# Kernel optimization log

Hardware: AMD Instinct MI355X
Metric: run time of the kernel (lower is better)

## Reference

```python
import jax, jax.numpy as jnp
import numpy as np

D_MODEL = 2048
H = 16
D_K = D_MODEL // H


def setup_inputs() -> dict:
    key = jax.random.key(0)
    ks = jax.random.split(key, 9)
    b, n, d = 2, 2048, D_MODEL
    s = 1.0 / np.sqrt(d)
    return {
        "x": jax.random.normal(ks[0], (b, n, d), jnp.float32),
        "Wq": jax.random.normal(ks[1], (d, d), jnp.float32) * s,
        "bq": jax.random.normal(ks[2], (d,), jnp.float32) * 0.01,
        "Wk": jax.random.normal(ks[3], (d, d), jnp.float32) * s,
        "bk": jax.random.normal(ks[4], (d,), jnp.float32) * 0.01,
        "Wv": jax.random.normal(ks[5], (d, d), jnp.float32) * s,
        "bv": jax.random.normal(ks[6], (d,), jnp.float32) * 0.01,
        "Wo": jax.random.normal(ks[7], (d, d), jnp.float32) * s,
        "bo": jax.random.normal(ks[8], (d,), jnp.float32) * 0.01,
    }


def reference(x, Wq, bq, Wk, bk, Wv, bv, Wo, bo):
    b, n, d = x.shape
    h, dk = H, D_K

    def split_heads(t):
        return t.reshape(b, n, h, dk).transpose(0, 2, 1, 3)  # (b,h,n,dk)

    q = split_heads(x @ Wq + bq)
    k = split_heads(x @ Wk + bk)
    v = split_heads(x @ Wv + bv)

    scores = jnp.einsum("bhqd,bhkd->bhqk", q, k) / jnp.sqrt(jnp.float32(dk))
    causal = jnp.tril(jnp.ones((n, n), dtype=bool))  # (n,n)
    scores = jnp.where(causal[None, None], scores, -jnp.inf)
    attn = jax.nn.softmax(scores, axis=-1)  # dropout = identity (eval)

    out = jnp.einsum("bhqk,bhkd->bhqd", attn, v)
    out = out.transpose(0, 2, 1, 3).reshape(b, n, d)
    return out @ Wo + bo
```

## Files before the change

kernel.cpp:

```cpp
#include <hip/hip_runtime.h>

typedef unsigned short u16;
typedef unsigned int u32;
typedef __attribute__((ext_vector_type(8))) short short8;
typedef __attribute__((ext_vector_type(4))) float f32x4;
typedef __attribute__((ext_vector_type(16))) float f32x16;
typedef __attribute__((ext_vector_type(4))) u16 u16x4;
typedef __attribute__((ext_vector_type(4))) u32 u32x4;

#define QK_SCALE 0.12751736915185197f

__device__ __forceinline__ u16 f2bf(float f) {
  u32 u = __builtin_bit_cast(u32, f);
  u = u + 0x7FFFu + ((u >> 16) & 1u);
  return (u16)(u >> 16);
}

__device__ __forceinline__ void async_copy16(const void* g, void* l) {
  __builtin_amdgcn_global_load_lds(
      (const __attribute__((address_space(1))) u32*)g,
      (__attribute__((address_space(3))) u32*)l, 16, 0, 0);
}

#define VMCNT(n) asm volatile("s_waitcnt vmcnt(" #n ")" ::: "memory")

__global__ __launch_bounds__(256) void cast_x_kernel(const float* __restrict__ x,
                                                     u16* __restrict__ xb, int n) {
  int i = (blockIdx.x * 256 + threadIdx.x) * 8;
  if (i >= n) return;
  float4 a = *(const float4*)(x + i);
  float4 b = *(const float4*)(x + i + 4);
  short8 o;
  o[0] = (short)f2bf(a.x); o[1] = (short)f2bf(a.y);
  o[2] = (short)f2bf(a.z); o[3] = (short)f2bf(a.w);
  o[4] = (short)f2bf(b.x); o[5] = (short)f2bf(b.y);
  o[6] = (short)f2bf(b.z); o[7] = (short)f2bf(b.w);
  *(short8*)(xb + i) = o;
}

__global__ __launch_bounds__(256) void transW_kernel(
    const float* __restrict__ W0, const float* __restrict__ W1,
    const float* __restrict__ W2, const float* __restrict__ W3,
    u16* __restrict__ O0, u16* __restrict__ O1, u16* __restrict__ O2, u16* __restrict__ O3) {
  const float* Ws[4] = {W0, W1, W2, W3};
  u16* Os[4] = {O0, O1, O2, O3};
  const float* W = Ws[blockIdx.z];
  u16* O = Os[blockIdx.z];

  __shared__ float T[64][65];
  int t = threadIdx.x;
  int k0 = blockIdx.y * 64, n0 = blockIdx.x * 64;
  int r = t >> 4, c = (t & 15) * 4;
#pragma unroll
  for (int i = 0; i < 4; ++i) {
    float4 v = *(const float4*)&W[(size_t)(k0 + r + i * 16) * 2048 + n0 + c];
    T[r + i * 16][c + 0] = v.x; T[r + i * 16][c + 1] = v.y;
    T[r + i * 16][c + 2] = v.z; T[r + i * 16][c + 3] = v.w;
  }
  __syncthreads();
#pragma unroll
  for (int i = 0; i < 4; ++i) {
    int nn = r + i * 16;
    u16x4 o;
    o[0] = f2bf(T[c + 0][nn]); o[1] = f2bf(T[c + 1][nn]);
    o[2] = f2bf(T[c + 2][nn]); o[3] = f2bf(T[c + 3][nn]);
    *(u16x4*)&O[(size_t)(n0 + nn) * 2048 + k0 + c] = o;
  }
}

__global__ __launch_bounds__(512, 2) void gemm192_kernel(
    const u16* __restrict__ A, const u16* __restrict__ W,
    const float* __restrict__ b0, const float* __restrict__ b1, const float* __restrict__ b2,
    u16* __restrict__ oq, u16* __restrict__ ok, u16* __restrict__ ovt) {
  __shared__ __align__(16) u16 SM[57344];

  int t = threadIdx.x;
  int lane = t & 63, w = t >> 6;
  int wm = w >> 2, wn = w & 3;
  int g = lane >> 4, lr = lane & 15;
  int m0 = blockIdx.y * 256, n0 = blockIdx.x * 192;

  const u16* AsrcB = A + (size_t)(m0 + (t >> 3)) * 2048 + ((t & 7) ^ ((t >> 3) & 7)) * 8;
  const u16* BsrcB = W + (size_t)(n0 + (t >> 3)) * 2048 + ((t & 7) ^ ((t >> 3) & 7)) * 8;
  int t8 = t * 8;

  int ko0 = (g ^ (lr & 7)) * 8;
  int ko1 = ((4 + g) ^ (lr & 7)) * 8;
  int aoff[8], boff[3];
#pragma unroll
  for (int mf = 0; mf < 8; ++mf) aoff[mf] = (wm * 128 + mf * 16 + lr) * 64;
#pragma unroll
  for (int nf = 0; nf < 3; ++nf) boff[nf] = 16384 + (wn * 48 + nf * 16 + lr) * 64;

  f32x4 acc[8][3] = {};
  short8 bfr[3][2];

#define SA(bb, j, tl) \
  async_copy16(AsrcB + (size_t)(j) * 131072 + (tl) * 64, (void*)(SM + (bb) * 28672 + (j) * 4096 + t8))
#define SB(bb, j, tl) \
  async_copy16(BsrcB + (size_t)(j) * 131072 + (tl) * 64, \
               (void*)(SM + (bb) * 28672 + 16384 + (j) * 4096 + t8))

#define PH(bufofs, half, STAGE_OPS, VM_OP)                                      \
  {                                                                             \
    const u16* Ab = SM + (bufofs);                                              \
    short8 af[4][2];                                                            \
    _Pragma("unroll") for (int mf = 0; mf < 4; ++mf) {                          \
      af[mf][0] = *(const short8*)&Ab[aoff[4 * (half) + mf] + ko0];             \
      af[mf][1] = *(const short8*)&Ab[aoff[4 * (half) + mf] + ko1];             \
    }                                                                           \
    if ((half) == 0) {                                                          \
      _Pragma("unroll") for (int nf = 0; nf < 3; ++nf) {                        \
        bfr[nf][0] = *(const short8*)&Ab[boff[nf] + ko0];                       \
        bfr[nf][1] = *(const short8*)&Ab[boff[nf] + ko1];                       \
      }                                                                         \
    }                                                                           \
    STAGE_OPS;                                                                  \
    asm volatile("s_waitcnt lgkmcnt(0)" ::: "memory");                          \
    __builtin_amdgcn_sched_barrier(0);                                          \
    __builtin_amdgcn_s_setprio(1);                                              \
    _Pragma("unroll") for (int kk = 0; kk < 2; ++kk)                            \
        _Pragma("unroll") for (int mf = 0; mf < 4; ++mf)                        \
            _Pragma("unroll") for (int nf = 0; nf < 3; ++nf)                    \
                acc[4 * (half) + mf][nf] = __builtin_amdgcn_mfma_f32_16x16x32_bf16(\
                    af[mf][kk], bfr[nf][kk], acc[4 * (half) + mf][nf], 0, 0, 0);\
    __builtin_amdgcn_s_setprio(0);                                              \
    VM_OP;                                                                      \
    __builtin_amdgcn_s_barrier();                                               \
  }

  SB(0, 0, 0); SB(0, 1, 0); SB(0, 2, 0);
  SA(0, 0, 0); SA(0, 1, 0); SA(0, 2, 0); SA(0, 3, 0);
  SB(1, 0, 1); SB(1, 1, 1); SB(1, 2, 1);
  SA(1, 0, 1); SA(1, 2, 1);
  VMCNT(5);
  __builtin_amdgcn_s_barrier();

  for (int i = 0; i < 16; ++i) {
    bool more = i < 15;
    int t1 = 2 * i + 1, t2 = 2 * i + 2, t3 = 2 * i + 3;
    PH(0, 0, { SA(1, 1, t1); SA(1, 3, t1); }, { VMCNT(7); });
    PH(0, 1,
       { if (more) { SB(0, 0, t2); SB(0, 1, t2); SB(0, 2, t2); SA(0, 0, t2); SA(0, 2, t2); } },
       { if (more) { VMCNT(7); } else { VMCNT(2); } });
    PH(28672, 0, { if (more) { SA(0, 1, t2); SA(0, 3, t2); } },
       { if (more) { VMCNT(7); } else { VMCNT(0); } });
    PH(28672, 1,
       { if (more) { SB(1, 0, t3); SB(1, 1, t3); SB(1, 2, t3); SA(1, 0, t3); SA(1, 2, t3); } },
       { if (more) { VMCNT(7); } });
  }
#undef PH
#undef SA
#undef SB

  bool hasV = (n0 + 191) >= 4096;
#pragma unroll
  for (int mf = 0; mf < 8; ++mf) {
#pragma unroll
    for (int nf = 0; nf < 3; ++nf) {
      int colc = wn * 48 + nf * 16 + lr;
      int col = n0 + colc;
      int z = col >> 11;
      int cc = col & 2047;
      if (z < 2) {
        float bv = (z == 0 ? b0 : b1)[cc];
        u16* outb = (z == 0) ? oq : ok;
#pragma unroll
        for (int i = 0; i < 4; ++i) {
          int rr = m0 + wm * 128 + mf * 16 + 4 * g + i;
          int b = rr >> 11, np = rr & 2047, h = cc >> 7, dk = cc & 127;
          outb[((size_t)(b * 16 + h) * 2048 + np) * 128 + dk] = f2bf(acc[mf][nf][i] + bv);
        }
      } else {
        float bv = b2[cc];
#pragma unroll
        for (int i = 0; i < 4; ++i) {
          int token = wm * 128 + mf * 16 + 4 * g + i;
          SM[colc * 264 + token] = f2bf(acc[mf][nf][i] + bv);
        }
      }
    }
  }
  if (hasV) {
    __syncthreads();
    int b = m0 >> 11;
    int npb = m0 & 2047;
#pragma unroll
    for (int it = 0; it < 12; ++it) {
      int id = t + 512 * it;
      int colc = id >> 5;
      int c8 = (id & 31) * 8;
      int col = n0 + colc;
      if (col >= 4096) {
        short8 v = *(const short8*)&SM[colc * 264 + c8];
        int vcol = col - 4096;
        int h = vcol >> 7, dk = vcol & 127;
        *(short8*)&ovt[(((size_t)(b * 16 + h) * 128 + dk) * 2048) + npb + c8] = v;
      }
    }
  }
}

__global__ __launch_bounds__(512, 2) void gemmO_kernel(
    const u16* __restrict__ A, const u16* __restrict__ W,
    const float* __restrict__ bias, float* __restrict__ of) {
  __shared__ __align__(16) u16 SM[73728];

  int t = threadIdx.x;
  int lane = t & 63, w = t >> 6;
  int wm = w >> 2, wn = w & 3;
  int g = lane >> 4, lr = lane & 15;
  int m0 = blockIdx.y * 128, n0 = blockIdx.x * 256;

  int sArow = ((t >> 8) << 6) + ((t >> 3) & 31);
  int c8A = (t & 7) ^ ((t >> 3) & 7);
  const u16* Asrc = A + (size_t)(m0 + sArow) * 2048 + c8A * 8;
  int rB = t >> 3;
  int c8B = (t & 7) ^ (rB & 7);
  const u16* Bsrc = W + (size_t)(n0 + rB) * 2048 + c8B * 8;

  int ko0 = (g ^ (lr & 7)) * 8;
  int ko1 = ((4 + g) ^ (lr & 7)) * 8;
  int offA[4], offB[4];
#pragma unroll
  for (int mf = 0; mf < 4; ++mf)
    offA[mf] = (mf >> 1) * 4096 + wm * 2048 + ((mf & 1) * 16 + lr) * 64;
#pragma unroll
  for (int nf = 0; nf < 4; ++nf)
    offB[nf] = 8192 + (wn >> 1) * 8192 + ((wn & 1) * 64 + nf * 16 + lr) * 64;

  f32x4 acc[4][4] = {};

#define STG_A(sbuf, mh, kt) \
  async_copy16(Asrc + (mh) * 65536 + (kt), (void*)(SM + (sbuf) + (mh) * 4096 + t * 8))
#define STG_B(sbuf, half, kt)                                                 \
  do {                                                                        \
    async_copy16(Bsrc + (half) * 262144 + (kt),                               \
                 (void*)(SM + (sbuf) + 8192 + (half) * 8192 + t * 8));        \
    async_copy16(Bsrc + (half) * 262144 + 131072 + (kt),                      \
                 (void*)(SM + (sbuf) + 8192 + (half) * 8192 + 4096 + t * 8)); \
  } while (0)

  STG_A(0, 0, 0); STG_B(0, 0, 0);
  STG_A(0, 1, 0); STG_B(0, 1, 0);
  STG_A(24576, 0, 64); STG_B(24576, 0, 64);
  STG_A(24576, 1, 64); STG_B(24576, 1, 64);
  VMCNT(6);
  __builtin_amdgcn_s_barrier();

  u32 cb = 0, sb = 49152;
  for (int tt = 0; tt < 32; ++tt) {
    int kt2 = (tt + 2) << 6;
    bool stg = tt < 30;
    const u16* Bu = SM + cb;

    short8 af[2][2], bfr[4][2];
#pragma unroll
    for (int m2 = 0; m2 < 2; ++m2) {
      af[m2][0] = *(const short8*)&Bu[offA[m2] + ko0];
      af[m2][1] = *(const short8*)&Bu[offA[m2] + ko1];
    }
#pragma unroll
    for (int nf = 0; nf < 4; ++nf) {
      bfr[nf][0] = *(const short8*)&Bu[offB[nf] + ko0];
      bfr[nf][1] = *(const short8*)&Bu[offB[nf] + ko1];
    }
    if (stg) { STG_A(sb, 0, kt2); STG_B(sb, 0, kt2); }
    __builtin_amdgcn_s_barrier();
    asm volatile("s_waitcnt lgkmcnt(0)" ::: "memory");
    __builtin_amdgcn_sched_barrier(0);
    __builtin_amdgcn_s_setprio(1);
#pragma unroll
    for (int kk = 0; kk < 2; ++kk)
#pragma unroll
      for (int m2 = 0; m2 < 2; ++m2)
#pragma unroll
        for (int nf = 0; nf < 4; ++nf)
          acc[m2][nf] =
              __builtin_amdgcn_mfma_f32_16x16x32_bf16(af[m2][kk], bfr[nf][kk], acc[m2][nf], 0, 0, 0);
    __builtin_amdgcn_s_setprio(0);
    __builtin_amdgcn_s_barrier();

#pragma unroll
    for (int m2 = 0; m2 < 2; ++m2) {
      af[m2][0] = *(const short8*)&Bu[offA[2 + m2] + ko0];
      af[m2][1] = *(const short8*)&Bu[offA[2 + m2] + ko1];
    }
    if (stg) { STG_A(sb, 1, kt2); STG_B(sb, 1, kt2); }
    __builtin_amdgcn_s_barrier();
    asm volatile("s_waitcnt lgkmcnt(0)" ::: "memory");
    __builtin_amdgcn_sched_barrier(0);
    __builtin_amdgcn_s_setprio(1);
#pragma unroll
    for (int kk = 0; kk < 2; ++kk)
#pragma unroll
      for (int m2 = 0; m2 < 2; ++m2)
#pragma unroll
        for (int nf = 0; nf < 4; ++nf)
          acc[2 + m2][nf] = __builtin_amdgcn_mfma_f32_16x16x32_bf16(af[m2][kk], bfr[nf][kk],
                                                                    acc[2 + m2][nf], 0, 0, 0);
    __builtin_amdgcn_s_setprio(0);
    if (tt < 30) { VMCNT(6); } else { VMCNT(0); }
    __builtin_amdgcn_s_barrier();

    cb += 24576; if (cb == 73728) cb = 0;
    sb += 24576; if (sb == 73728) sb = 0;
  }
#undef STG_A
#undef STG_B

#pragma unroll
  for (int mf = 0; mf < 4; ++mf) {
#pragma unroll
    for (int nf = 0; nf < 4; ++nf) {
      int col = n0 + wn * 64 + nf * 16 + lr;
      float bv = bias[col];
#pragma unroll
      for (int i = 0; i < 4; ++i) {
        int rr = m0 + wm * 64 + mf * 16 + 4 * g + i;
        of[(size_t)rr * 2048 + col] = acc[mf][nf][i] + bv;
      }
    }
  }
}

__global__ __launch_bounds__(256, 2) void attn_kernel(
    const u16* __restrict__ Q, const u16* __restrict__ K, const u16* __restrict__ Vt,
    u16* __restrict__ ctx) {
  int bh = blockIdx.y;
  int q0 = (int)(gridDim.x - 1 - blockIdx.x) * 128;
  int t = threadIdx.x, lane = t & 63, w = t >> 6;
  int h = lane >> 5;
  int ql = lane & 31;
  int q0w = q0 + w * 32;
  int qg = q0w + ql;

  const u16* Qb = Q + (size_t)bh * 262144;
  const u16* Kb = K + (size_t)bh * 262144;
  const u16* Vb = Vt + (size_t)bh * 262144;

  __shared__ __align__(16) u16 SM[32768];

  short8 qf[8];
  {
    const u16* qrow = Qb + (size_t)qg * 128 + 8 * h;
#pragma unroll
    for (int kk = 0; kk < 8; ++kk) qf[kk] = *(const short8*)(qrow + 16 * kk);
  }

  f32x16 acc[4] = {};
  float m = -1e30f, lsum = 0.f;

  int nt = (q0 + 128) >> 6;
  int wave_max = q0w + 31;

  auto STAGE = [&](int buf, int kv0) {
    u16* Ksb = SM + buf * 16384;
    u16* Vsb = Ksb + 8192;
#pragma unroll
    for (int it = 0; it < 4; ++it) {
      int p = t + 256 * it;
      int row = p >> 4;
      int c = (p & 15) ^ (row & 15);
      async_copy16(Kb + (size_t)(kv0 + row) * 128 + c * 8, (void*)(Ksb + p * 8));
      async_copy16(Vb + (size_t)(2 * row + (c >> 3)) * 2048 + kv0 + (c & 7) * 8,
                   (void*)(Vsb + p * 8));
    }
  };

  STAGE(0, 0);
  __syncthreads();

  for (int step = 0; step < nt; ++step) {
    int kv0 = step << 6;
    int cur = step & 1;
    if (step + 1 < nt) STAGE(cur ^ 1, (step + 1) << 6);

    if (kv0 <= wave_max) {
      const u16* Ksb = SM + cur * 16384;
      const u16* Vsb = Ksb + 8192;

      f32x16 s0 = {}, s1 = {};
      __builtin_amdgcn_s_setprio(1);
#pragma unroll
      for (int kk = 0; kk < 8; ++kk) {
        int c = (2 * kk + h) ^ (ql & 15);
        short8 kf0 = *(const short8*)&Ksb[ql * 128 + c * 8];
        s0 = __builtin_amdgcn_mfma_f32_32x32x16_bf16(kf0, qf[kk], s0, 0, 0, 0);
        short8 kf1 = *(const short8*)&Ksb[(32 + ql) * 128 + c * 8];
        s1 = __builtin_amdgcn_mfma_f32_32x32x16_bf16(kf1, qf[kk], s1, 0, 0, 0);
      }
      __builtin_amdgcn_s_setprio(0);

      if (kv0 + 63 > q0w) {
#pragma unroll
        for (int r = 0; r < 16; ++r) {
          int slot = (r & 3) + 8 * (r >> 2) + 4 * h;
          if (kv0 + slot > qg) s0[r] = -1e30f;
          if (kv0 + 32 + slot > qg) s1[r] = -1e30f;
        }
      }

      float tm = fmaxf(s0[0], s1[0]);
#pragma unroll
      for (int r = 1; r < 16; ++r) tm = fmaxf(tm, fmaxf(s0[r], s1[r]));
      tm = fmaxf(tm, __shfl_xor(tm, 32));
      tm *= QK_SCALE;

      if (__any(tm > m + 8.0f)) {
        float mn = fmaxf(m, tm);
        float rr = exp2f(m - mn);
        m = mn;
        lsum *= rr;
#pragma unroll
        for (int d = 0; d < 4; ++d)
#pragma unroll
          for (int i = 0; i < 16; ++i) acc[d][i] *= rr;
      }

      float rs = 0.f;
#pragma unroll
      for (int r = 0; r < 16; ++r) {
        s0[r] = exp2f(fmaf(s0[r], QK_SCALE, -m));
        s1[r] = exp2f(fmaf(s1[r], QK_SCALE, -m));
        rs += s0[r] + s1[r];
      }
      rs += __shfl_xor(rs, 32);
      lsum += rs;

      u32 up0[8], up1[8];
#pragma unroll
      for (int mi = 0; mi < 8; ++mi) {
        asm("v_cvt_pk_bf16_f32 %0, %1, %2" : "=v"(up0[mi]) : "v"(s0[2 * mi]), "v"(s0[2 * mi + 1]));
        asm("v_cvt_pk_bf16_f32 %0, %1, %2" : "=v"(up1[mi]) : "v"(s1[2 * mi]), "v"(s1[2 * mi + 1]));
      }

#pragma unroll
      for (int g16 = 0; g16 < 4; ++g16) {
        int Qd = g16 & 1;
        u32 c0 = (g16 < 2) ? up0[4 * Qd + 0] : up1[4 * Qd + 0];
        u32 c1 = (g16 < 2) ? up0[4 * Qd + 1] : up1[4 * Qd + 1];
        u32 c2 = (g16 < 2) ? up0[4 * Qd + 2] : up1[4 * Qd + 2];
        u32 c3 = (g16 < 2) ? up0[4 * Qd + 3] : up1[4 * Qd + 3];
        u32 d0 = __shfl_xor(c0, 32), d1 = __shfl_xor(c1, 32);
        u32 d2 = __shfl_xor(c2, 32), d3 = __shfl_xor(c3, 32);
        u32x4 paw;
        paw[0] = h ? d2 : c0;
        paw[1] = h ? d3 : c1;
        paw[2] = h ? c2 : d0;
        paw[3] = h ? c3 : d1;
        short8 pa = __builtin_bit_cast(short8, paw);
        __builtin_amdgcn_s_setprio(1);
#pragma unroll
        for (int d = 0; d < 4; ++d) {
          int dk = 32 * d + ql;
          int prow = dk >> 1;
          int lch = (dk & 1) * 8 + 2 * g16 + h;
          int slot = lch ^ (prow & 15);
          short8 vf = *(const short8*)&Vsb[prow * 128 + slot * 8];
          acc[d] = __builtin_amdgcn_mfma_f32_32x32x16_bf16(vf, pa, acc[d], 0, 0, 0);
        }
        __builtin_amdgcn_s_setprio(0);
      }
    }
    __syncthreads();
  }

  u16* Ot = SM + w * 4352;
  float inv = 1.f / lsum;
#pragma unroll
  for (int d = 0; d < 4; ++d)
#pragma unroll
    for (int r = 0; r < 16; ++r) {
      int dk = 32 * d + (r & 3) + 8 * (r >> 2) + 4 * h;
      Ot[ql * 136 + dk] = f2bf(acc[d][r] * inv);
    }
  __syncthreads();
  int b = bh >> 4, hh = bh & 15;
#pragma unroll
  for (int it = 0; it < 8; ++it) {
    int p = lane + 64 * it;
    int row = p >> 4, ch = p & 15;
    short8 v = *(const short8*)&Ot[row * 136 + ch * 8];
    *(short8*)(ctx + ((size_t)(b * 2048 + q0 + w * 32 + row)) * 2048 + hh * 128 + ch * 8) = v;
  }
}

extern "C" void kernel_launch(void* const* d_in, const int* in_sizes, int n_in,
                              void* d_out, int out_size, void* d_ws, size_t ws_size,
                              hipStream_t stream) {
  const float* x = (const float*)d_in[0];
  const float* Wq = (const float*)d_in[1];
  const float* bq = (const float*)d_in[2];
  const float* Wk = (const float*)d_in[3];
  const float* bk = (const float*)d_in[4];
  const float* Wv = (const float*)d_in[5];
  const float* bv = (const float*)d_in[6];
  const float* Wo = (const float*)d_in[7];
  const float* bo = (const float*)d_in[8];
  float* out = (float*)d_out;

  u16* xb = (u16*)d_ws;
  u16* WTq = xb + 8388608;
  u16* WTk = WTq + 4194304;
  u16* WTv = WTk + 4194304;
  u16* WTo = WTv + 4194304;
  u16* Qs = WTo + 4194304;
  u16* Ks = Qs + 8388608;
  u16* Vt = Ks + 8388608;
  u16* ctx = Vt + 8388608;

  cast_x_kernel<<<4096, 256, 0, stream>>>(x, xb, 8388608);
  transW_kernel<<<dim3(32, 32, 4), 256, 0, stream>>>(Wq, Wk, Wv, Wo, WTq, WTk, WTv, WTo);
  gemm192_kernel<<<dim3(32, 16), 512, 0, stream>>>(xb, WTq, bq, bk, bv, Qs, Ks, Vt);
  attn_kernel<<<dim3(16, 32), 256, 0, stream>>>(Qs, Ks, Vt, ctx);
  gemmO_kernel<<<dim3(8, 32), 512, 0, stream>>>(ctx, WTo, bo, out);
}
```

Before: 248.1 us.

## Split KV tiles across two wave groups per attention block and merge softmax states

After: 321.4 us. 1.3x slower.

```diff
diff --git a/kernel.cpp b/kernel.cpp
--- a/kernel.cpp
+++ b/kernel.cpp
@@ -324,15 +324,16 @@
   }
 }
 
-__global__ __launch_bounds__(256, 2) void attn_kernel(
+__global__ __launch_bounds__(512, 4) void attn_kernel(
     const u16* __restrict__ Q, const u16* __restrict__ K, const u16* __restrict__ Vt,
     u16* __restrict__ ctx) {
   int bh = blockIdx.y;
   int q0 = (int)(gridDim.x - 1 - blockIdx.x) * 128;
   int t = threadIdx.x, lane = t & 63, w = t >> 6;
+  int par = w >> 2;
   int h = lane >> 5;
   int ql = lane & 31;
-  int q0w = q0 + w * 32;
+  int q0w = q0 + (w & 3) * 32;
   int qg = q0w + ql;
 
   const u16* Qb = Q + (size_t)bh * 262144;
@@ -351,59 +352,59 @@
   f32x16 acc[4] = {};
   float m = -1e30f, lsum = 0.f;
 
-  int nt = (q0 + 128) >> 6;
+  int nt = (q0 + 128) >> 5;
   int wave_max = q0w + 31;
 
-  auto STAGE = [&](int buf, int kv0) {
-    u16* Ksb = SM + buf * 16384;
-    u16* Vsb = Ksb + 8192;
-#pragma unroll
-    for (int it = 0; it < 4; ++it) {
-      int p = t + 256 * it;
-      int row = p >> 4;
-      int c = (p & 15) ^ (row & 15);
-      async_copy16(Kb + (size_t)(kv0 + row) * 128 + c * 8, (void*)(Ksb + p * 8));
-      async_copy16(Vb + (size_t)(2 * row + (c >> 3)) * 2048 + kv0 + (c & 7) * 8,
-                   (void*)(Vsb + p * 8));
+  auto STAGE = [&](int s) {
+    int kv0 = s << 5;
+    u16* Ksb = SM + (s & 3) * 4096;
+    u16* Vsb = SM + 16384 + (s & 3) * 4096;
+    {
+      int row = t >> 4, c = (t & 15) ^ ((t >> 4) & 15);
+      async_copy16(Kb + (size_t)(kv0 + row) * 128 + c * 8, (void*)(Ksb + t * 8));
+    }
+    {
+      int row = t >> 3, lch = (t & 7) ^ ((t >> 3) & 7);
+      async_copy16(Vb + (size_t)(2 * row + (lch >> 2)) * 2048 + kv0 + (lch & 3) * 8,
+                   (void*)(Vsb + t * 8));
     }
   };
 
-  STAGE(0, 0);
-  __syncthreads();
-
-  for (int step = 0; step < nt; ++step) {
-    int kv0 = step << 6;
-    int cur = step & 1;
-    if (step + 1 < nt) STAGE(cur ^ 1, (step + 1) << 6);
+  STAGE(0); STAGE(1); STAGE(2); STAGE(3);
+
+  int nS = nt >> 1;
+  for (int S = 0; S < nS; ++S) {
+    int e = 2 * S + par;
+    int kv0 = e << 5;
+
+    if (S + 1 < nS) { VMCNT(4); } else { VMCNT(0); }
+    __builtin_amdgcn_s_barrier();
 
     if (kv0 <= wave_max) {
-      const u16* Ksb = SM + cur * 16384;
-      const u16* Vsb = Ksb + 8192;
-
-      f32x16 s0 = {}, s1 = {};
+      const u16* Ksb = SM + (e & 3) * 4096;
+      const u16* Vsb = SM + 16384 + (e & 3) * 4096;
+
+      f32x16 s = {};
       __builtin_amdgcn_s_setprio(1);
 #pragma unroll
       for (int kk = 0; kk < 8; ++kk) {
         int c = (2 * kk + h) ^ (ql & 15);
-        short8 kf0 = *(const short8*)&Ksb[ql * 128 + c * 8];
-        s0 = __builtin_amdgcn_mfma_f32_32x32x16_bf16(kf0, qf[kk], s0, 0, 0, 0);
-        short8 kf1 = *(const short8*)&Ksb[(32 + ql) * 128 + c * 8];
-        s1 = __builtin_amdgcn_mfma_f32_32x32x16_bf16(kf1, qf[kk], s1, 0, 0, 0);
+        short8 kf = *(const short8*)&Ksb[ql * 128 + c * 8];
+        s = __builtin_amdgcn_mfma_f32_32x32x16_bf16(kf, qf[kk], s, 0, 0, 0);
       }
       __builtin_amdgcn_s_setprio(0);
 
-      if (kv0 + 63 > q0w) {
+      if (kv0 + 31 > q0w) {
 #pragma unroll
         for (int r = 0; r < 16; ++r) {
           int slot = (r & 3) + 8 * (r >> 2) + 4 * h;
-          if (kv0 + slot > qg) s0[r] = -1e30f;
-          if (kv0 + 32 + slot > qg) s1[r] = -1e30f;
+          if (kv0 + slot > qg) s[r] = -1e30f;
         }
       }
 
-      float tm = fmaxf(s0[0], s1[0]);
-#pragma unroll
-      for (int r = 1; r < 16; ++r) tm = fmaxf(tm, fmaxf(s0[r], s1[r]));
+      float tm = s[0];
+#pragma unroll
+      for (int r = 1; r < 16; ++r) tm = fmaxf(tm, s[r]);
       tm = fmaxf(tm, __shfl_xor(tm, 32));
       tm *= QK_SCALE;
 
@@ -421,27 +422,21 @@
       float rs = 0.f;
 #pragma unroll
       for (int r = 0; r < 16; ++r) {
-        s0[r] = exp2f(fmaf(s0[r], QK_SCALE, -m));
-        s1[r] = exp2f(fmaf(s1[r], QK_SCALE, -m));
-        rs += s0[r] + s1[r];
+        s[r] = exp2f(fmaf(s[r], QK_SCALE, -m));
+        rs += s[r];
       }
       rs += __shfl_xor(rs, 32);
       lsum += rs;
 
-      u32 up0[8], up1[8];
-#pragma unroll
-      for (int mi = 0; mi < 8; ++mi) {
-        asm("v_cvt_pk_bf16_f32 %0, %1, %2" : "=v"(up0[mi]) : "v"(s0[2 * mi]), "v"(s0[2 * mi + 1]));
-        asm("v_cvt_pk_bf16_f32 %0, %1, %2" : "=v"(up1[mi]) : "v"(s1[2 * mi]), "v"(s1[2 * mi + 1]));
-      }
-
-#pragma unroll
-      for (int g16 = 0; g16 < 4; ++g16) {
-        int Qd = g16 & 1;
-        u32 c0 = (g16 < 2) ? up0[4 * Qd + 0] : up1[4 * Qd + 0];
-        u32 c1 = (g16 < 2) ? up0[4 * Qd + 1] : up1[4 * Qd + 1];
-        u32 c2 = (g16 < 2) ? up0[4 * Qd + 2] : up1[4 * Qd + 2];
-        u32 c3 = (g16 < 2) ? up0[4 * Qd + 3] : up1[4 * Qd + 3];
+      u32 up[8];
+#pragma unroll
+      for (int mi = 0; mi < 8; ++mi)
+        asm("v_cvt_pk_bf16_f32 %0, %1, %2" : "=v"(up[mi]) : "v"(s[2 * mi]), "v"(s[2 * mi + 1]));
+
+#pragma unroll
+      for (int g16 = 0; g16 < 2; ++g16) {
+        u32 c0 = up[4 * g16 + 0], c1 = up[4 * g16 + 1];
+        u32 c2 = up[4 * g16 + 2], c3 = up[4 * g16 + 3];
         u32 d0 = __shfl_xor(c0, 32), d1 = __shfl_xor(c1, 32);
         u32 d2 = __shfl_xor(c2, 32), d3 = __shfl_xor(c3, 32);
         u32x4 paw;
@@ -455,34 +450,78 @@
         for (int d = 0; d < 4; ++d) {
           int dk = 32 * d + ql;
           int prow = dk >> 1;
-          int lch = (dk & 1) * 8 + 2 * g16 + h;
-          int slot = lch ^ (prow & 15);
-          short8 vf = *(const short8*)&Vsb[prow * 128 + slot * 8];
+          int lch = (dk & 1) * 4 + 2 * g16 + h;
+          int slot = lch ^ (prow & 7);
+          short8 vf = *(const short8*)&Vsb[prow * 64 + slot * 8];
           acc[d] = __builtin_amdgcn_mfma_f32_32x32x16_bf16(vf, pa, acc[d], 0, 0, 0);
         }
         __builtin_amdgcn_s_setprio(0);
       }
     }
-    __syncthreads();
-  }
-
-  u16* Ot = SM + w * 4352;
-  float inv = 1.f / lsum;
-#pragma unroll
-  for (int d = 0; d < 4; ++d)
+
+    __builtin_amdgcn_s_barrier();
+    if (S + 2 < nS) { STAGE(2 * S + 4); STAGE(2 * S + 5); }
+  }
+
+  __syncthreads();
+  float* MF = (float*)SM;
+  float* my = MF + (w & 3) * 4096 + lane * 36;
+  if (par) {
+    my[0] = m; my[1] = lsum;
+#pragma unroll
+    for (int r = 0; r < 16; ++r) { my[2 + r] = acc[0][r]; my[18 + r] = acc[1][r]; }
+  }
+  __syncthreads();
+  float fa = 1.f, fb = 0.f, lst = lsum;
+  if (!par) {
+    float mb = my[0], lb = my[1];
+    float ms = fmaxf(m, mb);
+    fa = exp2f(m - ms);
+    fb = exp2f(mb - ms);
+    lst = lsum * fa + lb * fb;
 #pragma unroll
     for (int r = 0; r < 16; ++r) {
-      int dk = 32 * d + (r & 3) + 8 * (r >> 2) + 4 * h;
-      Ot[ql * 136 + dk] = f2bf(acc[d][r] * inv);
-    }
-  __syncthreads();
-  int b = bh >> 4, hh = bh & 15;
-#pragma unroll
-  for (int it = 0; it < 8; ++it) {
-    int p = lane + 64 * it;
-    int row = p >> 4, ch = p & 15;
-    short8 v = *(const short8*)&Ot[row * 136 + ch * 8];
-    *(short8*)(ctx + ((size_t)(b * 2048 + q0 + w * 32 + row)) * 2048 + hh * 128 + ch * 8) = v;
+      acc[0][r] = acc[0][r] * fa + my[2 + r] * fb;
+      acc[1][r] = acc[1][r] * fa + my[18 + r] * fb;
+    }
+  }
+  __syncthreads();
+  if (par) {
+#pragma unroll
+    for (int r = 0; r < 16; ++r) { my[2 + r] = acc[2][r]; my[18 + r] = acc[3][r]; }
+  }
+  __syncthreads();
+  if (!par) {
+#pragma unroll
+    for (int r = 0; r < 16; ++r) {
+      acc[2][r] = acc[2][r] * fa + my[2 + r] * fb;
+      acc[3][r] = acc[3][r] * fa + my[18 + r] * fb;
+    }
+  }
+  __syncthreads();
+
+  if (!par) {
+    u16* Ot = SM + w * 4352;
+    float inv = 1.f / lst;
+#pragma unroll
+    for (int d = 0; d < 4; ++d)
+#pragma unroll
+      for (int r = 0; r < 16; ++r) {
+        int dk = 32 * d + (r & 3) + 8 * (r >> 2) + 4 * h;
+        Ot[ql * 136 + dk] = f2bf(acc[d][r] * inv);
+      }
+  }
+  __syncthreads();
+  if (!par) {
+    u16* Ot = SM + w * 4352;
+    int b = bh >> 4, hh = bh & 15;
+#pragma unroll
+    for (int it = 0; it < 8; ++it) {
+      int p = lane + 64 * it;
+      int row = p >> 4, ch = p & 15;
+      short8 v = *(const short8*)&Ot[row * 136 + ch * 8];
+      *(short8*)(ctx + ((size_t)(b * 2048 + q0 + w * 32 + row)) * 2048 + hh * 128 + ch * 8) = v;
+    }
   }
 }
 
@@ -513,6 +552,6 @@
   cast_x_kernel<<<4096, 256, 0, stream>>>(x, xb, 8388608);
   transW_kernel<<<dim3(32, 32, 4), 256, 0, stream>>>(Wq, Wk, Wv, Wo, WTq, WTk, WTv, WTo);
   gemm192_kernel<<<dim3(32, 16), 512, 0, stream>>>(xb, WTq, bq, bk, bv, Qs, Ks, Vt);
-  attn_kernel<<<dim3(16, 32), 256, 0, stream>>>(Qs, Ks, Vt, ctx);
+  attn_kernel<<<dim3(16, 32), 512, 0, stream>>>(Qs, Ks, Vt, ctx);
   gemmO_kernel<<<dim3(8, 32), 512, 0, stream>>>(ctx, WTo, bo, out);
 }
```
